# Kernel tuning notes

Measured on AMD Instinct MI355X. Metric: run time of the kernel, lower is better.

## Reference

```python
import jax, jax.numpy as jnp
import numpy as np

N_NODES = 100000
N_EDGES = 600000
NUM_RELS = 6
NUM_BASES = 6
DIMS = [26, 64, 128, 32]  # in_features -> hidden[0] -> hidden[1] -> X_dim


def _layer(h, etypes, src, dst, V, C, S, b):
    """One basis-decomposed RGCN layer (DGL RelGraphConv semantics).
    h: [N, in]; V: [num_bases, in, out]; C: [num_rels, num_bases];
    S: self-loop weight [in, out]; b: bias [out].
    """
    # compose relation weights from bases: [num_rels, in, out]
    W = jnp.einsum('rb,bio->rio', C, V)
    # transform every node by every relation (cheaper than per-edge [E,in,out])
    h_rel = jnp.einsum('ni,rio->rno', h, W)          # [num_rels, N, out]
    msg = h_rel[etypes, src]                          # [E, out] gather
    agg = jax.ops.segment_sum(msg, dst, num_segments=h.shape[0])  # scatter-add
    return jax.nn.relu(agg + h @ S + b)


def setup_inputs() -> dict:
    key = jax.random.key(0)
    ks = jax.random.split(key, 16)
    inp = {
        'node_feats': jax.random.normal(ks[0], (N_NODES, DIMS[0]), dtype=jnp.float32),
        'src': jax.random.randint(ks[1], (N_EDGES,), 0, N_NODES, dtype=jnp.int32),
        'dst': jax.random.randint(ks[2], (N_EDGES,), 0, N_NODES, dtype=jnp.int32),
        'etypes': jax.random.randint(ks[3], (N_EDGES,), 0, NUM_RELS, dtype=jnp.int32),
    }
    ki = 4
    for l in range(3):
        din, dout = DIMS[l], DIMS[l + 1]
        sc = 1.0 / np.sqrt(din)
        inp[f'V{l+1}'] = jax.random.normal(ks[ki], (NUM_BASES, din, dout), dtype=jnp.float32) * sc
        inp[f'C{l+1}'] = jax.random.normal(ks[ki+1], (NUM_RELS, NUM_BASES), dtype=jnp.float32) * (1.0 / np.sqrt(NUM_BASES))
        inp[f'S{l+1}'] = jax.random.normal(ks[ki+2], (din, dout), dtype=jnp.float32) * sc
        inp[f'b{l+1}'] = jnp.zeros((dout,), dtype=jnp.float32)
        ki += 3
    return inp


def reference(node_feats, src, dst, etypes,
              V1, C1, S1, b1, V2, C2, S2, b2, V3, C3, S3, b3):
    h = _layer(node_feats, etypes, src, dst, V1, C1, S1, b1)
    h = _layer(h, etypes, src, dst, V2, C2, S2, b2)
    h = _layer(h, etypes, src, dst, V3, C3, S3, b3)
    return h
```

## Files before the change

kernel.cpp:

```cpp
#include <hip/hip_runtime.h>

#define NN 100000
#define NE 600000
#define NR 6
#define NB 6
#define NKEY (NN * NR)
#define NCHUNK ((NKEY + 1023) / 1024)

typedef __attribute__((ext_vector_type(8))) short bfrag;
typedef __attribute__((ext_vector_type(8))) unsigned short uvec8;
typedef __attribute__((ext_vector_type(4))) float accvec;

__device__ __forceinline__ float bf2f(unsigned short u) {
  union { unsigned int i; float f; } v;
  v.i = ((unsigned int)u) << 16;
  return v.f;
}
__device__ __forceinline__ unsigned short f2bf(float f) {
  union { float f; unsigned int i; } v;
  v.f = f;
  return (unsigned short)((v.i + 0x7FFFu + ((v.i >> 16) & 1u)) >> 16);
}

__global__ void pad_feats_bf16(const float* __restrict__ nf, unsigned short* __restrict__ hp) {
  int idx = blockIdx.x * 256 + threadIdx.x;
  if (idx >= NN * 4) return;
  int n = idx >> 2, c = idx & 3;
  uvec8 o;
#pragma unroll
  for (int i = 0; i < 8; ++i) {
    int k = c * 8 + i;
    o[i] = (k < 26) ? f2bf(nf[n * 26 + k]) : (unsigned short)0;
  }
  *(uvec8*)&hp[(size_t)n * 32 + c * 8] = o;
}

__global__ void hist2(const int* __restrict__ dst, const int* __restrict__ et,
                      int* __restrict__ cnt) {
  int e = blockIdx.x * 256 + threadIdx.x;
  if (e < NE) atomicAdd(&cnt[dst[e] * NR + et[e]], 1);
}

__global__ void scanA(const int* __restrict__ cnt, int* __restrict__ partial) {
  __shared__ int ts[256];
  int t = threadIdx.x;
  int base = blockIdx.x * 1024 + t * 4;
  int s = 0;
#pragma unroll
  for (int i = 0; i < 4; ++i)
    if (base + i < NKEY) s += cnt[base + i];
  ts[t] = s;
  __syncthreads();
  for (int off = 128; off; off >>= 1) {
    if (t < off) ts[t] += ts[t + off];
    __syncthreads();
  }
  if (t == 0) partial[blockIdx.x] = ts[0];
}

__global__ void scanB(int* __restrict__ partial) {
  __shared__ int ts[256];
  int t = threadIdx.x;
  int b = t * 3;
  int v[3], s = 0;
#pragma unroll
  for (int i = 0; i < 3; ++i) {
    v[i] = (b + i < NCHUNK) ? partial[b + i] : 0;
    s += v[i];
  }
  ts[t] = s;
  __syncthreads();
  for (int off = 1; off < 256; off <<= 1) {
    int x = (t >= off) ? ts[t - off] : 0;
    __syncthreads();
    ts[t] += x;
    __syncthreads();
  }
  int run = ts[t] - s;
#pragma unroll
  for (int i = 0; i < 3; ++i) {
    int tmp = v[i];
    if (b + i < NCHUNK) partial[b + i] = run;
    run += tmp;
  }
}

__global__ void scanC(int* __restrict__ cnt, const int* __restrict__ partial,
                      int* __restrict__ indptr, int* __restrict__ cur) {
  __shared__ int ts[256];
  int t = threadIdx.x;
  int base = blockIdx.x * 1024 + t * 4;
  int v[4], s = 0;
#pragma unroll
  for (int i = 0; i < 4; ++i) {
    v[i] = (base + i < NKEY) ? cnt[base + i] : 0;
    s += v[i];
  }
  ts[t] = s;
  __syncthreads();
  for (int off = 1; off < 256; off <<= 1) {
    int x = (t >= off) ? ts[t - off] : 0;
    __syncthreads();
    ts[t] += x;
    __syncthreads();
  }
  int run = partial[blockIdx.x] + ts[t] - s;
#pragma unroll
  for (int i = 0; i < 4; ++i) {
    if (base + i < NKEY) {
      indptr[base + i] = run;
      cur[base + i] = run;
      run += v[i];
    }
  }
  if (blockIdx.x == 0 && t == 0) indptr[NKEY] = NE;
}

__global__ void scatter2(const int* __restrict__ et, const int* __restrict__ src,
                         const int* __restrict__ dst, int* __restrict__ cur,
                         int* __restrict__ sidx, int* __restrict__ gidx) {
  int e = blockIdx.x * 256 + threadIdx.x;
  if (e < NE) {
    int r = et[e];
    int s = src[e];
    int key = dst[e] * NR + r;
    int pos = atomicAdd(&cur[key], 1);
    sidx[pos] = s;
    gidx[pos] = r * NN + s;
  }
}

template <int IN, int OUT, int KS, int NT>
__global__ void compose_wf(const float* __restrict__ V, const float* __restrict__ C,
                           const float* __restrict__ S, unsigned short* __restrict__ Wf) {
  int idx = blockIdx.x * 256 + threadIdx.x;
  if (idx >= (NR + 1) * KS * NT * 64) return;
  int lane = idx & 63;
  int t = idx >> 6;
  int nt = t % NT; t /= NT;
  int ks = t % KS; int rel = t / KS;
  int n = nt * 16 + (lane & 15);
  int g = lane >> 4;
  uvec8 o;
#pragma unroll
  for (int i = 0; i < 8; ++i) {
    int k = ks * 32 + g * 8 + i;
    float s = 0.f;
    if (k < IN) {
      if (rel < NR) {
#pragma unroll
        for (int b = 0; b < NB; ++b) s += C[rel * NB + b] * V[((size_t)b * IN + k) * OUT + n];
      } else {
        s = S[(size_t)k * OUT + n];
      }
    }
    o[i] = f2bf(s);
  }
  *(uvec8*)&Wf[(size_t)idx * 8] = o;
}

template <int K, int OUT, int MAXE, int BPEU>
__global__ __launch_bounds__(256, BPEU) void rgcn_layer_v5(
    const unsigned short* __restrict__ h,
    const unsigned short* __restrict__ Wf,
    const float* __restrict__ bias,
    const int* __restrict__ indptr,
    const int* __restrict__ sidx,
    unsigned short* __restrict__ Gout) {
  constexpr int ROWS = 16;
  constexpr int KS = K / 32;
  constexpr int KT = 7 * KS;
  constexpr int NT = OUT / 16;
  constexpr int NTW = NT / 4;
  constexpr int KC = K / 8;
  constexpr int CT = 7 * KC;
  constexpr int ITEMS = (ROWS * CT + 255) / 256;
  constexpr int KP = 7 * K + 8;
  constexpr int MSTRIDE = K + 8;
  constexpr int LDSE = (ROWS * KP > MAXE * MSTRIDE) ? ROWS * KP : MAXE * MSTRIDE;
  constexpr int SITER = MAXE * KC / 256;

  __shared__ unsigned short A[LDSE];
  __shared__ int seg[ROWS * NR + 1];

  const int tid = threadIdx.x;
  const int row0 = blockIdx.x * ROWS;

  if (tid < ROWS * NR + 1) seg[tid] = indptr[row0 * NR + tid];
  __syncthreads();

  const int E0 = seg[0];
  const int E1 = seg[ROWS * NR];

  float sum[ITEMS][8];
#pragma unroll
  for (int i = 0; i < ITEMS; ++i)
#pragma unroll
    for (int q = 0; q < 8; ++q) sum[i][q] = 0.f;

  for (int b0 = E0; b0 < E1; b0 += MAXE) {
    const int bcount = min(MAXE, E1 - b0);
    __syncthreads();

#pragma unroll
    for (int i = 0; i < SITER; ++i) {
      int idx = tid + i * 256;
      int e = idx / KC;
      int c = idx & (KC - 1);
      int ec = min(e, bcount - 1);
      int s = sidx[b0 + ec];
      *(uvec8*)&A[e * MSTRIDE + c * 8] = *(const uvec8*)&h[(size_t)s * K + c * 8];
    }
    __syncthreads();

#pragma unroll
    for (int i = 0; i < ITEMS; ++i) {
      int idx = tid + i * 256;
      if (idx < ROWS * CT) {
        int row = idx / CT, chunk = idx % CT;
        if (chunk < 6 * KC) {
          int rel = chunk / KC, c = chunk & (KC - 1);
          int beg = seg[row * NR + rel], end = seg[row * NR + rel + 1];
          int lo = max(beg, b0), hi = min(end, b0 + bcount);
          for (int e = lo; e < hi; ++e) {
            uvec8 t = *(const uvec8*)&A[(e - b0) * MSTRIDE + c * 8];
#pragma unroll
            for (int q = 0; q < 8; ++q) sum[i][q] += bf2f(t[q]);
          }
        }
      }
    }
  }

  __syncthreads();

#pragma unroll
  for (int i = 0; i < ITEMS; ++i) {
    int idx = tid + i * 256;
    if (idx < ROWS * CT) {
      int row = idx / CT, chunk = idx % CT;
      uvec8 o;
      if (chunk >= 6 * KC) {
        int c = chunk - 6 * KC;
        o = *(const uvec8*)&h[(size_t)(row0 + row) * K + c * 8];
      } else {
#pragma unroll
        for (int q = 0; q < 8; ++q) o[q] = f2bf(sum[i][q]);
      }
      *(uvec8*)&A[row * KP + chunk * 8] = o;
    }
  }
  __syncthreads();

  const int lane = tid & 63;
  const int wv = tid >> 6;
  const int abase = (lane & 15) * KP + (lane >> 4) * 8;

  accvec acc[NTW];
#pragma unroll
  for (int j = 0; j < NTW; ++j) acc[j] = 0.f;

#pragma unroll
  for (int kst = 0; kst < KT; ++kst) {
    bfrag af = *(const bfrag*)&A[abase + kst * 32];
#pragma unroll
    for (int j = 0; j < NTW; ++j) {
      int nt = wv * NTW + j;
      bfrag bf = *(const bfrag*)&Wf[(size_t)((kst * NT + nt) * 64 + lane) * 8];
      acc[j] = __builtin_amdgcn_mfma_f32_16x16x32_bf16(af, bf, acc[j], 0, 0, 0);
    }
  }

  const int r0 = row0 + (lane >> 4) * 4;
  const int col0 = lane & 15;
#pragma unroll
  for (int j = 0; j < NTW; ++j) {
    int c = (wv * NTW + j) * 16 + col0;
    float bv = bias[c];
#pragma unroll
    for (int r = 0; r < 4; ++r) {
      float v = fmaxf(acc[j][r] + bv, 0.f);
      Gout[(size_t)(r0 + r) * OUT + c] = f2bf(v);
    }
  }
}

template <int K, int OUT>
__global__ __launch_bounds__(256, 4) void rgcn_transform(
    const unsigned short* __restrict__ h,
    const unsigned short* __restrict__ Wf,
    unsigned short* __restrict__ Y) {
  constexpr int KS = K / 32;
  constexpr int NT = OUT / 16;
  constexpr int KC = K / 8;
  constexpr int KP = K + 8;

  __shared__ unsigned short Asm[64 * KP];
  const int tid = threadIdx.x;
  const int row0 = blockIdx.x * 64;

  for (int idx = tid; idx < 64 * KC; idx += 256) {
    int j = idx / KC, c = idx - (idx / KC) * KC;
    int row = row0 + j;
    uvec8 o = 0;
    if (row < NN) o = *(const uvec8*)&h[(size_t)row * K + c * 8];
    *(uvec8*)&Asm[j * KP + c * 8] = o;
  }
  __syncthreads();

  const int lane = tid & 63;
  const int wv = tid >> 6;
  const int abase = (wv * 16 + (lane & 15)) * KP + (lane >> 4) * 8;

  bfrag af[KS];
#pragma unroll
  for (int ks = 0; ks < KS; ++ks) af[ks] = *(const bfrag*)&Asm[abase + ks * 32];

  const int r0 = row0 + wv * 16 + (lane >> 4) * 4;
  const int col0 = lane & 15;

  for (int rel = 0; rel <= NR; ++rel) {
    accvec acc[NT];
#pragma unroll
    for (int nt = 0; nt < NT; ++nt) acc[nt] = 0.f;
    const unsigned short* Wr = Wf + (size_t)rel * KS * NT * 512;
#pragma unroll
    for (int ks = 0; ks < KS; ++ks) {
#pragma unroll
      for (int nt = 0; nt < NT; ++nt) {
        bfrag bf = *(const bfrag*)&Wr[(size_t)((ks * NT + nt) * 64 + lane) * 8];
        acc[nt] = __builtin_amdgcn_mfma_f32_16x16x32_bf16(af[ks], bf, acc[nt], 0, 0, 0);
      }
    }
#pragma unroll
    for (int nt = 0; nt < NT; ++nt) {
      int c = nt * 16 + col0;
#pragma unroll
      for (int r = 0; r < 4; ++r) {
        int row = r0 + r;
        if (row < NN)
          Y[((size_t)rel * NN + row) * OUT + c] = f2bf(acc[nt][r]);
      }
    }
  }
}

__global__ __launch_bounds__(256, 8) void rgcn_agg3(
    const unsigned short* __restrict__ Y,
    const int* __restrict__ indptr,
    const int* __restrict__ gidx,
    const float* __restrict__ bias,
    float* __restrict__ out) {
  int t = blockIdx.x * 256 + threadIdx.x;
  int row = t >> 2;
  if (row >= NN) return;
  int c = (t & 3) * 8;

  int beg = indptr[row * NR];
  int end = indptr[row * NR + NR];

  float s[8] = {0.f, 0.f, 0.f, 0.f, 0.f, 0.f, 0.f, 0.f};
  int e = beg;
  for (; e + 3 < end; e += 4) {
    int g0 = gidx[e], g1 = gidx[e + 1], g2 = gidx[e + 2], g3 = gidx[e + 3];
    uvec8 v0 = *(const uvec8*)&Y[(size_t)g0 * 32 + c];
    uvec8 v1 = *(const uvec8*)&Y[(size_t)g1 * 32 + c];
    uvec8 v2 = *(const uvec8*)&Y[(size_t)g2 * 32 + c];
    uvec8 v3 = *(const uvec8*)&Y[(size_t)g3 * 32 + c];
#pragma unroll
    for (int i = 0; i < 8; ++i)
      s[i] += (bf2f(v0[i]) + bf2f(v1[i])) + (bf2f(v2[i]) + bf2f(v3[i]));
  }
  for (; e < end; ++e) {
    int g = gidx[e];
    uvec8 v = *(const uvec8*)&Y[(size_t)g * 32 + c];
#pragma unroll
    for (int i = 0; i < 8; ++i) s[i] += bf2f(v[i]);
  }
  uvec8 vs = *(const uvec8*)&Y[((size_t)NR * NN + row) * 32 + c];
#pragma unroll
  for (int i = 0; i < 8; ++i) s[i] += bf2f(vs[i]);

  float4 o0, o1;
  o0.x = fmaxf(s[0] + bias[c + 0], 0.f);
  o0.y = fmaxf(s[1] + bias[c + 1], 0.f);
  o0.z = fmaxf(s[2] + bias[c + 2], 0.f);
  o0.w = fmaxf(s[3] + bias[c + 3], 0.f);
  o1.x = fmaxf(s[4] + bias[c + 4], 0.f);
  o1.y = fmaxf(s[5] + bias[c + 5], 0.f);
  o1.z = fmaxf(s[6] + bias[c + 6], 0.f);
  o1.w = fmaxf(s[7] + bias[c + 7], 0.f);
  *(float4*)&out[(size_t)row * 32 + c] = o0;
  *(float4*)&out[(size_t)row * 32 + c + 4] = o1;
}

static inline char* align_up(char* p, size_t a) {
  return (char*)(((size_t)p + a - 1) & ~(a - 1));
}

extern "C" void kernel_launch(void* const* d_in, const int* in_sizes, int n_in,
                              void* d_out, int out_size, void* d_ws, size_t ws_size,
                              hipStream_t stream) {
  const float* nf = (const float*)d_in[0];
  const int* src  = (const int*)d_in[1];
  const int* dst  = (const int*)d_in[2];
  const int* et   = (const int*)d_in[3];
  const float* V1 = (const float*)d_in[4];
  const float* C1 = (const float*)d_in[5];
  const float* S1 = (const float*)d_in[6];
  const float* b1 = (const float*)d_in[7];
  const float* V2 = (const float*)d_in[8];
  const float* C2 = (const float*)d_in[9];
  const float* S2 = (const float*)d_in[10];
  const float* b2 = (const float*)d_in[11];
  const float* V3 = (const float*)d_in[12];
  const float* C3 = (const float*)d_in[13];
  const float* S3 = (const float*)d_in[14];
  const float* b3 = (const float*)d_in[15];
  float* out = (float*)d_out;

  constexpr int WF1 = (NR + 1) * 1 * 4 * 512;
  constexpr int WF2 = (NR + 1) * 2 * 8 * 512;
  constexpr int WF3 = (NR + 1) * 4 * 2 * 512;

  char* p = (char*)d_ws;
  int* cnt = (int*)p;                p = align_up(p + (size_t)NKEY * 4, 256);
  int* indptr = (int*)p;             p = align_up(p + (size_t)(NKEY + 1) * 4, 256);
  int* partial = (int*)p;            p = align_up(p + (size_t)NCHUNK * 4, 256);
  int* sidx = (int*)p;               p = align_up(p + (size_t)NE * 4, 256);
  int* gidx = (int*)p;               p = align_up(p + (size_t)NE * 4, 256);
  unsigned short* hp = (unsigned short*)p;  p = align_up(p + (size_t)NN * 32 * 2, 256);
  unsigned short* W1 = (unsigned short*)p;  p = align_up(p + (size_t)WF1 * 2, 256);
  unsigned short* W2 = (unsigned short*)p;  p = align_up(p + (size_t)WF2 * 2, 256);
  unsigned short* W3 = (unsigned short*)p;  p = align_up(p + (size_t)WF3 * 2, 256);
  unsigned short* G1 = (unsigned short*)p;  p = align_up(p + (size_t)NN * 64 * 2, 256);
  unsigned short* G2 = (unsigned short*)p;  p = align_up(p + (size_t)NN * 128 * 2, 256);
  unsigned short* Y3 = (unsigned short*)p;  p = align_up(p + (size_t)(NR + 1) * NN * 32 * 2, 256);

  hipMemsetAsync(cnt, 0, (size_t)NKEY * 4, stream);

  const int EB = (NE + 255) / 256;
  pad_feats_bf16<<<(NN * 4 + 255) / 256, 256, 0, stream>>>(nf, hp);
  hist2<<<EB, 256, 0, stream>>>(dst, et, cnt);
  scanA<<<NCHUNK, 256, 0, stream>>>(cnt, partial);
  scanB<<<1, 256, 0, stream>>>(partial);
  scanC<<<NCHUNK, 256, 0, stream>>>(cnt, partial, indptr, cnt);
  scatter2<<<EB, 256, 0, stream>>>(et, src, dst, cnt, sidx, gidx);

  compose_wf<26, 64, 1, 4><<<(WF1 / 8 + 255) / 256, 256, 0, stream>>>(V1, C1, S1, W1);
  compose_wf<64, 128, 2, 8><<<(WF2 / 8 + 255) / 256, 256, 0, stream>>>(V2, C2, S2, W2);
  compose_wf<128, 32, 4, 2><<<(WF3 / 8 + 255) / 256, 256, 0, stream>>>(V3, C3, S3, W3);

  const int NB16 = NN / 16;
  rgcn_layer_v5<32, 64, 128, 8><<<NB16, 256, 0, stream>>>(hp, W1, b1, indptr, sidx, G1);
  rgcn_layer_v5<64, 128, 128, 8><<<NB16, 256, 0, stream>>>(G1, W2, b2, indptr, sidx, G2);

  const int NBK = (NN + 63) / 64;
  rgcn_transform<128, 32><<<NBK, 256, 0, stream>>>(G2, W3, Y3);
  rgcn_agg3<<<(NN * 4 + 255) / 256, 256, 0, stream>>>(Y3, indptr, gidx, b3, out);

  (void)in_sizes; (void)n_in; (void)out_size; (void)ws_size;
}
```

Before: 205.0 us.

## Store layer-1 activations in FP8 and fuse prep kernels and scan passes

Layer-1 output G1 is written in FP8 (e4m3 via the cvt builtins) instead of bf16, so layer 2 gathers half the bytes per neighbour row. The padding, histogram and three weight-compose kernels are merged into one launch, and the scan's middle pass is folded into the final pass, which now recomputes its block's prefix from the partial sums. This cuts gather traffic and launch count, but FP8 loses precision on hidden activations and each scan block redundantly sums up to ~586 partials.

```diff
diff --git a/kernel.cpp b/kernel.cpp
--- a/kernel.cpp
+++ b/kernel.cpp
@@ -9,6 +9,7 @@
 
 typedef __attribute__((ext_vector_type(8))) short bfrag;
 typedef __attribute__((ext_vector_type(8))) unsigned short uvec8;
+typedef __attribute__((ext_vector_type(8))) unsigned char ucvec8;
 typedef __attribute__((ext_vector_type(4))) float accvec;
 
 __device__ __forceinline__ float bf2f(unsigned short u) {
@@ -21,24 +22,76 @@
   v.f = f;
   return (unsigned short)((v.i + 0x7FFFu + ((v.i >> 16) & 1u)) >> 16);
 }
-
-__global__ void pad_feats_bf16(const float* __restrict__ nf, unsigned short* __restrict__ hp) {
-  int idx = blockIdx.x * 256 + threadIdx.x;
-  if (idx >= NN * 4) return;
-  int n = idx >> 2, c = idx & 3;
+__device__ __forceinline__ float fp82f(unsigned char u) {
+  return __builtin_amdgcn_cvt_f32_fp8((unsigned int)u, 0);
+}
+__device__ __forceinline__ unsigned char f2fp8(float f) {
+  return (unsigned char)(__builtin_amdgcn_cvt_pk_fp8_f32(f, 0.f, 0, false) & 0xff);
+}
+
+template <int IN, int OUT, int KS, int NT>
+__device__ __forceinline__ void compose_body(int idx, const float* __restrict__ V,
+                                             const float* __restrict__ C,
+                                             const float* __restrict__ S,
+                                             unsigned short* __restrict__ Wf) {
+  int lane = idx & 63;
+  int t = idx >> 6;
+  int nt = t % NT; t /= NT;
+  int ks = t % KS; int rel = t / KS;
+  int n = nt * 16 + (lane & 15);
+  int g = lane >> 4;
   uvec8 o;
 #pragma unroll
   for (int i = 0; i < 8; ++i) {
-    int k = c * 8 + i;
-    o[i] = (k < 26) ? f2bf(nf[n * 26 + k]) : (unsigned short)0;
-  }
-  *(uvec8*)&hp[(size_t)n * 32 + c * 8] = o;
-}
-
-__global__ void hist2(const int* __restrict__ dst, const int* __restrict__ et,
-                      int* __restrict__ cnt) {
-  int e = blockIdx.x * 256 + threadIdx.x;
-  if (e < NE) atomicAdd(&cnt[dst[e] * NR + et[e]], 1);
+    int k = ks * 32 + g * 8 + i;
+    float s = 0.f;
+    if (k < IN) {
+      if (rel < NR) {
+#pragma unroll
+        for (int b = 0; b < NB; ++b) s += C[rel * NB + b] * V[((size_t)b * IN + k) * OUT + n];
+      } else {
+        s = S[(size_t)k * OUT + n];
+      }
+    }
+    o[i] = f2bf(s);
+  }
+  *(uvec8*)&Wf[(size_t)idx * 8] = o;
+}
+
+#define PB_PAD 1563
+#define PB_HIST 2344
+__global__ __launch_bounds__(256) void prep_kernel(
+    const float* __restrict__ nf, unsigned short* __restrict__ hp,
+    const int* __restrict__ dst, const int* __restrict__ et, int* __restrict__ cnt,
+    const float* V1, const float* C1, const float* S1, unsigned short* W1,
+    const float* V2, const float* C2, const float* S2, unsigned short* W2,
+    const float* V3, const float* C3, const float* S3, unsigned short* W3) {
+  int b = blockIdx.x, tid = threadIdx.x;
+  if (b < PB_PAD) {
+    int idx = b * 256 + tid;
+    if (idx < NN * 4) {
+      int n = idx >> 2, c = idx & 3;
+      uvec8 o;
+#pragma unroll
+      for (int i = 0; i < 8; ++i) {
+        int k = c * 8 + i;
+        o[i] = (k < 26) ? f2bf(nf[n * 26 + k]) : (unsigned short)0;
+      }
+      *(uvec8*)&hp[(size_t)n * 32 + c * 8] = o;
+    }
+  } else if (b < PB_PAD + PB_HIST) {
+    int e = (b - PB_PAD) * 256 + tid;
+    if (e < NE) atomicAdd(&cnt[dst[e] * NR + et[e]], 1);
+  } else if (b < PB_PAD + PB_HIST + 7) {
+    int idx = (b - PB_PAD - PB_HIST) * 256 + tid;
+    compose_body<26, 64, 1, 4>(idx, V1, C1, S1, W1);
+  } else if (b < PB_PAD + PB_HIST + 7 + 28) {
+    int idx = (b - PB_PAD - PB_HIST - 7) * 256 + tid;
+    compose_body<64, 128, 2, 8>(idx, V2, C2, S2, W2);
+  } else {
+    int idx = (b - PB_PAD - PB_HIST - 35) * 256 + tid;
+    compose_body<128, 32, 4, 2>(idx, V3, C3, S3, W3);
+  }
 }
 
 __global__ void scanA(const int* __restrict__ cnt, int* __restrict__ partial) {
@@ -58,14 +111,27 @@
   if (t == 0) partial[blockIdx.x] = ts[0];
 }
 
-__global__ void scanB(int* __restrict__ partial) {
+__global__ void scanC2(int* __restrict__ cnt, const int* __restrict__ partial,
+                       int* __restrict__ indptr) {
   __shared__ int ts[256];
   int t = threadIdx.x;
-  int b = t * 3;
-  int v[3], s = 0;
-#pragma unroll
-  for (int i = 0; i < 3; ++i) {
-    v[i] = (b + i < NCHUNK) ? partial[b + i] : 0;
+  int bid = blockIdx.x;
+  int ps = 0;
+  for (int i = t; i < bid; i += 256) ps += partial[i];
+  ts[t] = ps;
+  __syncthreads();
+  for (int off = 128; off; off >>= 1) {
+    if (t < off) ts[t] += ts[t + off];
+    __syncthreads();
+  }
+  int base = ts[0];
+  __syncthreads();
+
+  int bbase = bid * 1024 + t * 4;
+  int v[4], s = 0;
+#pragma unroll
+  for (int i = 0; i < 4; ++i) {
+    v[i] = (bbase + i < NKEY) ? cnt[bbase + i] : 0;
     s += v[i];
   }
   ts[t] = s;
@@ -76,44 +142,16 @@
     ts[t] += x;
     __syncthreads();
   }
-  int run = ts[t] - s;
-#pragma unroll
-  for (int i = 0; i < 3; ++i) {
-    int tmp = v[i];
-    if (b + i < NCHUNK) partial[b + i] = run;
-    run += tmp;
-  }
-}
-
-__global__ void scanC(int* __restrict__ cnt, const int* __restrict__ partial,
-                      int* __restrict__ indptr, int* __restrict__ cur) {
-  __shared__ int ts[256];
-  int t = threadIdx.x;
-  int base = blockIdx.x * 1024 + t * 4;
-  int v[4], s = 0;
+  int run = base + ts[t] - s;
 #pragma unroll
   for (int i = 0; i < 4; ++i) {
-    v[i] = (base + i < NKEY) ? cnt[base + i] : 0;
-    s += v[i];
-  }
-  ts[t] = s;
-  __syncthreads();
-  for (int off = 1; off < 256; off <<= 1) {
-    int x = (t >= off) ? ts[t - off] : 0;
-    __syncthreads();
-    ts[t] += x;
-    __syncthreads();
-  }
-  int run = partial[blockIdx.x] + ts[t] - s;
-#pragma unroll
-  for (int i = 0; i < 4; ++i) {
-    if (base + i < NKEY) {
-      indptr[base + i] = run;
-      cur[base + i] = run;
+    if (bbase + i < NKEY) {
+      indptr[bbase + i] = run;
+      cnt[bbase + i] = run;
       run += v[i];
     }
   }
-  if (blockIdx.x == 0 && t == 0) indptr[NKEY] = NE;
+  if (bid == 0 && t == 0) indptr[NKEY] = NE;
 }
 
 __global__ void scatter2(const int* __restrict__ et, const int* __restrict__ src,
@@ -130,43 +168,14 @@
   }
 }
 
-template <int IN, int OUT, int KS, int NT>
-__global__ void compose_wf(const float* __restrict__ V, const float* __restrict__ C,
-                           const float* __restrict__ S, unsigned short* __restrict__ Wf) {
-  int idx = blockIdx.x * 256 + threadIdx.x;
-  if (idx >= (NR + 1) * KS * NT * 64) return;
-  int lane = idx & 63;
-  int t = idx >> 6;
-  int nt = t % NT; t /= NT;
-  int ks = t % KS; int rel = t / KS;
-  int n = nt * 16 + (lane & 15);
-  int g = lane >> 4;
-  uvec8 o;
-#pragma unroll
-  for (int i = 0; i < 8; ++i) {
-    int k = ks * 32 + g * 8 + i;
-    float s = 0.f;
-    if (k < IN) {
-      if (rel < NR) {
-#pragma unroll
-        for (int b = 0; b < NB; ++b) s += C[rel * NB + b] * V[((size_t)b * IN + k) * OUT + n];
-      } else {
-        s = S[(size_t)k * OUT + n];
-      }
-    }
-    o[i] = f2bf(s);
-  }
-  *(uvec8*)&Wf[(size_t)idx * 8] = o;
-}
-
-template <int K, int OUT, int MAXE, int BPEU>
-__global__ __launch_bounds__(256, BPEU) void rgcn_layer_v5(
-    const unsigned short* __restrict__ h,
+template <int K, int OUT, int MAXE, bool IN_FP8, bool OUT_FP8>
+__global__ __launch_bounds__(256, 8) void rgcn_layer_v6(
+    const void* __restrict__ hv,
     const unsigned short* __restrict__ Wf,
     const float* __restrict__ bias,
     const int* __restrict__ indptr,
     const int* __restrict__ sidx,
-    unsigned short* __restrict__ Gout) {
+    void* __restrict__ Gout) {
   constexpr int ROWS = 16;
   constexpr int KS = K / 32;
   constexpr int KT = 7 * KS;
@@ -176,12 +185,15 @@
   constexpr int CT = 7 * KC;
   constexpr int ITEMS = (ROWS * CT + 255) / 256;
   constexpr int KP = 7 * K + 8;
-  constexpr int MSTRIDE = K + 8;
-  constexpr int LDSE = (ROWS * KP > MAXE * MSTRIDE) ? ROWS * KP : MAXE * MSTRIDE;
+  constexpr int MSB = IN_FP8 ? (K + 8) : (2 * K + 16);
+  constexpr int ATB = ROWS * KP * 2;
+  constexpr int MGB = MAXE * MSB;
+  constexpr int LDSB = ATB > MGB ? ATB : MGB;
   constexpr int SITER = MAXE * KC / 256;
 
-  __shared__ unsigned short A[LDSE];
+  __shared__ __align__(16) char buf[LDSB];
   __shared__ int seg[ROWS * NR + 1];
+  unsigned short* A = (unsigned short*)buf;
 
   const int tid = threadIdx.x;
   const int row0 = blockIdx.x * ROWS;
@@ -209,7 +221,13 @@
       int c = idx & (KC - 1);
       int ec = min(e, bcount - 1);
       int s = sidx[b0 + ec];
-      *(uvec8*)&A[e * MSTRIDE + c * 8] = *(const uvec8*)&h[(size_t)s * K + c * 8];
+      if constexpr (IN_FP8) {
+        *(ucvec8*)&buf[e * MSB + c * 8] =
+            *(const ucvec8*)((const unsigned char*)hv + (size_t)s * K + c * 8);
+      } else {
+        *(uvec8*)&buf[e * MSB + c * 16] =
+            *(const uvec8*)((const unsigned short*)hv + (size_t)s * K + c * 8);
+      }
     }
     __syncthreads();
 
@@ -223,9 +241,15 @@
           int beg = seg[row * NR + rel], end = seg[row * NR + rel + 1];
           int lo = max(beg, b0), hi = min(end, b0 + bcount);
           for (int e = lo; e < hi; ++e) {
-            uvec8 t = *(const uvec8*)&A[(e - b0) * MSTRIDE + c * 8];
-#pragma unroll
-            for (int q = 0; q < 8; ++q) sum[i][q] += bf2f(t[q]);
+            if constexpr (IN_FP8) {
+              ucvec8 t = *(const ucvec8*)&buf[(e - b0) * MSB + c * 8];
+#pragma unroll
+              for (int q = 0; q < 8; ++q) sum[i][q] += fp82f(t[q]);
+            } else {
+              uvec8 t = *(const uvec8*)&buf[(e - b0) * MSB + c * 16];
+#pragma unroll
+              for (int q = 0; q < 8; ++q) sum[i][q] += bf2f(t[q]);
+            }
           }
         }
       }
@@ -242,7 +266,14 @@
       uvec8 o;
       if (chunk >= 6 * KC) {
         int c = chunk - 6 * KC;
-        o = *(const uvec8*)&h[(size_t)(row0 + row) * K + c * 8];
+        if constexpr (IN_FP8) {
+          ucvec8 tv = *(const ucvec8*)((const unsigned char*)hv +
+                                       (size_t)(row0 + row) * K + c * 8);
+#pragma unroll
+          for (int q = 0; q < 8; ++q) o[q] = f2bf(fp82f(tv[q]));
+        } else {
+          o = *(const uvec8*)((const unsigned short*)hv + (size_t)(row0 + row) * K + c * 8);
+        }
       } else {
 #pragma unroll
         for (int q = 0; q < 8; ++q) o[q] = f2bf(sum[i][q]);
@@ -280,7 +311,10 @@
 #pragma unroll
     for (int r = 0; r < 4; ++r) {
       float v = fmaxf(acc[j][r] + bv, 0.f);
-      Gout[(size_t)(r0 + r) * OUT + c] = f2bf(v);
+      if constexpr (OUT_FP8)
+        ((unsigned char*)Gout)[(size_t)(r0 + r) * OUT + c] = f2fp8(v);
+      else
+        ((unsigned short*)Gout)[(size_t)(r0 + r) * OUT + c] = f2bf(v);
     }
   }
 }
@@ -433,27 +467,24 @@
   unsigned short* W1 = (unsigned short*)p;  p = align_up(p + (size_t)WF1 * 2, 256);
   unsigned short* W2 = (unsigned short*)p;  p = align_up(p + (size_t)WF2 * 2, 256);
   unsigned short* W3 = (unsigned short*)p;  p = align_up(p + (size_t)WF3 * 2, 256);
-  unsigned short* G1 = (unsigned short*)p;  p = align_up(p + (size_t)NN * 64 * 2, 256);
+  unsigned char* G1 = (unsigned char*)p;    p = align_up(p + (size_t)NN * 64, 256);
   unsigned short* G2 = (unsigned short*)p;  p = align_up(p + (size_t)NN * 128 * 2, 256);
   unsigned short* Y3 = (unsigned short*)p;  p = align_up(p + (size_t)(NR + 1) * NN * 32 * 2, 256);
 
   hipMemsetAsync(cnt, 0, (size_t)NKEY * 4, stream);
 
   const int EB = (NE + 255) / 256;
-  pad_feats_bf16<<<(NN * 4 + 255) / 256, 256, 0, stream>>>(nf, hp);
-  hist2<<<EB, 256, 0, stream>>>(dst, et, cnt);
+  prep_kernel<<<PB_PAD + PB_HIST + 49, 256, 0, stream>>>(
+      nf, hp, dst, et, cnt, V1, C1, S1, W1, V2, C2, S2, W2, V3, C3, S3, W3);
   scanA<<<NCHUNK, 256, 0, stream>>>(cnt, partial);
-  scanB<<<1, 256, 0, stream>>>(partial);
-  scanC<<<NCHUNK, 256, 0, stream>>>(cnt, partial, indptr, cnt);
+  scanC2<<<NCHUNK, 256, 0, stream>>>(cnt, partial, indptr);
   scatter2<<<EB, 256, 0, stream>>>(et, src, dst, cnt, sidx, gidx);
 
-  compose_wf<26, 64, 1, 4><<<(WF1 / 8 + 255) / 256, 256, 0, stream>>>(V1, C1, S1, W1);
-  compose_wf<64, 128, 2, 8><<<(WF2 / 8 + 255) / 256, 256, 0, stream>>>(V2, C2, S2, W2);
-  compose_wf<128, 32, 4, 2><<<(WF3 / 8 + 255) / 256, 256, 0, stream>>>(V3, C3, S3, W3);
-
   const int NB16 = NN / 16;
-  rgcn_layer_v5<32, 64, 128, 8><<<NB16, 256, 0, stream>>>(hp, W1, b1, indptr, sidx, G1);
-  rgcn_layer_v5<64, 128, 128, 8><<<NB16, 256, 0, stream>>>(G1, W2, b2, indptr, sidx, G2);
+  rgcn_layer_v6<32, 64, 128, false, true><<<NB16, 256, 0, stream>>>(
+      hp, W1, b1, indptr, sidx, G1);
+  rgcn_layer_v6<64, 128, 128, true, false><<<NB16, 256, 0, stream>>>(
+      G1, W2, b2, indptr, sidx, G2);
 
   const int NBK = (NN + 63) / 64;
   rgcn_transform<128, 32><<<NBK, 256, 0, stream>>>(G2, W3, Y3);
```

New measurement: 184.1 us. 10.2% less time.
